# Kernel optimization log

Measured on AMD Instinct MI355X. Metric: run time of the kernel, lower is better.

## Reference

```python
import jax, jax.numpy as jnp
import numpy as np

EPS = 1e-6

def rmsnorm(x, w):
    # matches torch RMSNorm: normalize in fp32, cast back, scale
    xf = x.astype(jnp.float32)
    n = xf * jax.lax.rsqrt(jnp.mean(xf * xf, axis=-1, keepdims=True) + EPS)
    return n.astype(x.dtype) * w

def swiglu(x, w1, w2, w3):
    # torch Linear convention: weight shape [out, in], y = x @ W.T
    return (jax.nn.silu(x @ w1.T) * (x @ w3.T)) @ w2.T

B, D, E, K = 32768, 1024, 8, 2
NF = 4  # int(8 * 0.5) fractal experts, rest are plain SwiGLU(dim, 4*dim)

def setup_inputs() -> dict:
    key = jax.random.key(0)
    ks = jax.random.split(key, 8)
    def w(k, shape, fan_in):
        return jax.random.normal(k, shape, jnp.float32) * (fan_in ** -0.5)
    return {
        "x": jax.random.normal(ks[0], (B, D), jnp.float32),
        "gate_w": w(ks[1], (E, D), D),
        # FractalBlock experts (depth=1): RMSNorm weight, SwiGLU(dim, 2*dim), LayerScale gamma
        "fr_norm": jnp.ones((NF, D), jnp.float32),
        "fr_gamma": jnp.full((NF, D), 1e-5, jnp.float32),
        "fr_w1": w(ks[2], (NF, 2 * D, D), D),
        "fr_w2": w(ks[3], (NF, D, 2 * D), 2 * D),
        "fr_w3": w(ks[4], (NF, 2 * D, D), D),
        # Plain SwiGLU experts: SwiGLU(dim, 4*dim)
        "sw_w1": w(ks[5], (E - NF, 4 * D, D), D),
        "sw_w2": w(ks[6], (E - NF, D, 4 * D), 4 * D),
        "sw_w3": w(ks[7], (E - NF, 4 * D, D), D),
    }

def reference(x, gate_w, fr_norm, fr_gamma, fr_w1, fr_w2, fr_w3, sw_w1, sw_w2, sw_w3):
    n_experts = gate_w.shape[0]
    n_fractal = fr_w1.shape[0]
    # gating: softmax -> top-k -> renormalize selected weights
    probs = jax.nn.softmax(x @ gate_w.T, axis=-1)            # [B, E]
    tk_w, tk_i = jax.lax.top_k(probs, K)                     # [B, K]
    tk_w = tk_w / jnp.sum(tk_w, axis=-1, keepdims=True)
    # combine weights: zero for unselected experts (math identical to sparse dispatch)
    comb = jnp.sum(jax.nn.one_hot(tk_i, n_experts, dtype=x.dtype) * tk_w[..., None], axis=1)  # [B, E]
    out = jnp.zeros_like(x)
    for e in range(n_experts):  # fixed small structural loop over experts
        if e < n_fractal:
            # FractalBlock(depth=1), eval mode: stochastic depth is identity
            xn = rmsnorm(x, fr_norm[e])
            xn = xn + swiglu(xn, fr_w1[e], fr_w2[e], fr_w3[e])
            eo = fr_gamma[e] * xn + x
        else:
            j = e - n_fractal
            eo = swiglu(x, sw_w1[j], sw_w2[j], sw_w3[j])
        out = out + comb[:, e:e + 1] * eo
    return out
```

## Files before the change

### kernel.cpp

```cpp
#include <hip/hip_runtime.h>
#include <stdint.h>

#define B_TOK 32768
#define DIM   1024
#define NEXP  8
#define NFR   4
#define HF    2048
#define HS    4096
#define CT1   32
#define CT2   64
#define NCH   9
#define PADROWS 67584

typedef __bf16 bf16;
typedef bf16  bf16x8 __attribute__((ext_vector_type(8)));
typedef bf16  bf16x4 __attribute__((ext_vector_type(4)));
typedef float f32x4  __attribute__((ext_vector_type(4)));

#define LDSOFF(R, CC) (((R) << 6) + ((((CC) ^ ((R) & 7))) << 3))

__global__ __launch_bounds__(256) void gate_kernel(
    const float* __restrict__ x, const float* __restrict__ gw_g,
    bf16* __restrict__ xb, float* __restrict__ rms,
    int* __restrict__ top2, float* __restrict__ c12) {
  __shared__ float gw[NEXP * DIM];
  for (int i = threadIdx.x; i < NEXP * DIM / 4; i += 256)
    *(f32x4*)(gw + i * 4) = *(const f32x4*)(gw_g + i * 4);
  __syncthreads();
  const int lane = threadIdx.x & 63;
  const int wave = threadIdx.x >> 6;
  const int row  = blockIdx.x * 4 + wave;
  const float* xr = x + (size_t)row * DIM;
  f32x4 xv[4];
#pragma unroll
  for (int i = 0; i < 4; i++) xv[i] = *(const f32x4*)(xr + lane * 4 + i * 256);
  float ss = 0.f;
  double dot[8] = {0, 0, 0, 0, 0, 0, 0, 0};
#pragma unroll
  for (int i = 0; i < 4; i++) {
#pragma unroll
    for (int c = 0; c < 4; c++) ss += xv[i][c] * xv[i][c];
#pragma unroll
    for (int e = 0; e < 8; e++) {
      const f32x4 g = *(const f32x4*)(gw + e * DIM + i * 256 + lane * 4);
#pragma unroll
      for (int c = 0; c < 4; c++) dot[e] += (double)xv[i][c] * (double)g[c];
    }
  }
#pragma unroll
  for (int off = 32; off > 0; off >>= 1) {
    ss += __shfl_xor(ss, off, 64);
#pragma unroll
    for (int e = 0; e < 8; e++) dot[e] += __shfl_xor(dot[e], off, 64);
  }
  const float rv = 1.0f / sqrtf(ss * (1.0f / DIM) + 1e-6f);
  if (lane == 0) rms[row] = rv;
  int i1 = 0; double m1 = dot[0];
#pragma unroll
  for (int e = 1; e < 8; e++) if (dot[e] > m1) { m1 = dot[e]; i1 = e; }
  int i2 = 0; double m2 = -1e300;
#pragma unroll
  for (int e = 0; e < 8; e++) if (e != i1 && dot[e] > m2) { m2 = dot[e]; i2 = e; }
  const double t  = exp(m2 - m1);
  if (lane == 0) {
    top2[row] = i1 | (i2 << 8);
    c12[2 * row]     = (float)(1.0 / (1.0 + t));
    c12[2 * row + 1] = (float)(t / (1.0 + t));
  }
#pragma unroll
  for (int i = 0; i < 4; i++) {
    bf16x4 o;
#pragma unroll
    for (int c = 0; c < 4; c++) o[c] = (bf16)xv[i][c];
    *(bf16x4*)(xb + (size_t)row * DIM + lane * 4 + i * 256) = o;
  }
}

__global__ __launch_bounds__(1024) void histoff_kernel(
    const int* __restrict__ top2, int* __restrict__ tileOff256,
    int* __restrict__ tileOff128, int* __restrict__ rowOff) {
  __shared__ int h[8];
  if (threadIdx.x < 8) h[threadIdx.x] = 0;
  __syncthreads();
  int c[8] = {0, 0, 0, 0, 0, 0, 0, 0};
  for (int i = 0; i < B_TOK / 1024; i++) {
    const int pk = top2[threadIdx.x + i * 1024];
    const int e1 = pk & 255, e2 = pk >> 8;
#pragma unroll
    for (int e = 0; e < 8; e++) c[e] += (e1 == e) + (e2 == e);
  }
#pragma unroll
  for (int e = 0; e < 8; e++) {
#pragma unroll
    for (int off = 32; off > 0; off >>= 1) c[e] += __shfl_xor(c[e], off, 64);
  }
  if ((threadIdx.x & 63) == 0) {
#pragma unroll
    for (int e = 0; e < 8; e++) atomicAdd(&h[e], c[e]);
  }
  __syncthreads();
  if (threadIdx.x == 0) {
    int t = 0;
    for (int e = 0; e < 8; e++) {
      tileOff256[e] = t;
      tileOff128[e] = 2 * t;
      rowOff[e]     = t * 256;
      t += (h[e] + 255) >> 8;
    }
    tileOff256[8] = t;
    tileOff128[8] = 2 * t;
  }
}

__global__ __launch_bounds__(256) void assign_kernel(
    const int* __restrict__ top2, const float* __restrict__ c12,
    const int* __restrict__ rowOff, int* __restrict__ cur,
    int* __restrict__ perm, float* __restrict__ cwg) {
  __shared__ int lhist[8];
  __shared__ int lbase[8];
  if (threadIdx.x < 8) lhist[threadIdx.x] = 0;
  __syncthreads();
  const int t = blockIdx.x * 256 + threadIdx.x;
  const int pk = top2[t];
  const int e1 = pk & 255, e2 = pk >> 8;
  const int p1 = atomicAdd(&lhist[e1], 1);
  const int p2 = atomicAdd(&lhist[e2], 1);
  __syncthreads();
  if (threadIdx.x < 8) {
    const int c = lhist[threadIdx.x];
    lbase[threadIdx.x] = c ? atomicAdd(&cur[threadIdx.x * 32], c) : 0;
  }
  __syncthreads();
  const int g1 = rowOff[e1] + lbase[e1] + p1;
  perm[g1] = t; cwg[g1] = c12[2 * t];
  const int g2 = rowOff[e2] + lbase[e2] + p2;
  perm[g2] = t; cwg[g2] = c12[2 * t + 1];
}

__global__ __launch_bounds__(256) void cvt_kernel(
    const float* __restrict__ src, bf16* __restrict__ dst, int n4) {
  const int i = blockIdx.x * 256 + threadIdx.x;
  if (i >= n4) return;
  f32x4 v = *(const f32x4*)(src + (size_t)i * 4);
  *(bf16x4*)(dst + (size_t)i * 4) = __builtin_convertvector(v, bf16x4);
}

__global__ __launch_bounds__(256) void cvt_inter_fr(
    const float* __restrict__ w1, const float* __restrict__ w3,
    const float* __restrict__ norm, bf16* __restrict__ dst) {
  const int i = blockIdx.x * 256 + threadIdx.x;
  const int col4 = i & 255;
  const int rp   = (i >> 8) & 4095;
  const int e    = i >> 20;
  const int blk  = rp >> 4;
  const int sr   = ((blk >> 1) << 4) + (rp & 15);
  const float* src = (blk & 1) ? w3 : w1;
  f32x4 v  = *(const f32x4*)(src + ((size_t)e * HF + sr) * DIM + col4 * 4);
  f32x4 nv = *(const f32x4*)(norm + e * DIM + col4 * 4);
#pragma unroll
  for (int c = 0; c < 4; c++) v[c] *= nv[c];
  *(bf16x4*)(dst + ((size_t)e * 4096 + rp) * DIM + col4 * 4) =
      __builtin_convertvector(v, bf16x4);
}

__global__ __launch_bounds__(256) void cvt_inter_sw(
    const float* __restrict__ w1, const float* __restrict__ w3,
    bf16* __restrict__ dst) {
  const int i = blockIdx.x * 256 + threadIdx.x;
  const int col4 = i & 255;
  const int rp   = (i >> 8) & 8191;
  const int e    = i >> 21;
  const int blk  = rp >> 4;
  const int sr   = ((blk >> 1) << 4) + (rp & 15);
  const float* src = (blk & 1) ? w3 : w1;
  f32x4 v = *(const f32x4*)(src + ((size_t)e * HS + sr) * DIM + col4 * 4);
  *(bf16x4*)(dst + ((size_t)e * 8192 + rp) * DIM + col4 * 4) =
      __builtin_convertvector(v, bf16x4);
}

__device__ __forceinline__ void stage_sw(const bf16* __restrict__ g0, int ld,
                                         bf16* s0, int wave, int lane) {
  const int r = lane >> 3;
  const int c = (lane & 7) ^ r;
  const bf16* g = g0 + (size_t)(wave * 32 + r) * ld + c * 8;
  bf16* s = s0 + wave * 2048;
#pragma unroll
  for (int i = 0; i < 4; i++) {
    __builtin_amdgcn_global_load_lds(
        (const __attribute__((address_space(1))) void*)(uintptr_t)(g + (size_t)(i * 8) * ld),
        (__attribute__((address_space(3))) void*)(uintptr_t)(s + i * 512), 16, 0, 0);
  }
}

__global__ __launch_bounds__(512, 2) void gemm1_kernel(
    const bf16* __restrict__ xb, const int* __restrict__ perm,
    const float* __restrict__ rms,
    const bf16* __restrict__ fwi, const bf16* __restrict__ swi,
    const int* __restrict__ tileOff256, bf16* __restrict__ G, int chunk) {
  const int bt = chunk * CT1 + blockIdx.y;
  int toff[9];
#pragma unroll
  for (int i = 0; i < 9; i++) toff[i] = tileOff256[i];
  if (bt >= toff[8]) return;
  int e = 0;
#pragma unroll
  for (int i = 1; i < 8; i++) if (bt >= toff[i]) e = i;
  const bool isfr = (e < NFR);
  const int nt = isfr ? 16 : 32;
  if ((int)blockIdx.x >= nt) return;
  const bf16* Bp = isfr ? fwi + (size_t)e * 4096 * DIM
                        : swi + (size_t)(e - NFR) * 8192 * DIM;

  __shared__ __attribute__((aligned(16))) bf16 As[2 * 16384];
  __shared__ __attribute__((aligned(16))) bf16 Bs[2 * 16384];
  const int lane = threadIdx.x & 63, wave = threadIdx.x >> 6;
  const int wm = wave >> 2, wn = wave & 3;
  const int g0  = bt * 256;
  const int n0p = blockIdx.x * 256;

  const int rA = lane >> 3;
  const int cA = (lane & 7) ^ rA;
  const bf16* Ag[4];
#pragma unroll
  for (int i = 0; i < 4; i++) {
    int tk = perm[g0 + wave * 32 + i * 8 + rA];
    if (tk < 0) tk = 0;
    Ag[i] = xb + (size_t)tk * DIM + cA * 8;
  }
  const bf16* Bg = Bp + (size_t)(n0p + wave * 32 + rA) * DIM + cA * 8;

  f32x4 acc[8][4];
#pragma unroll
  for (int i = 0; i < 8; i++)
#pragma unroll
    for (int j = 0; j < 4; j++) { f32x4 z = {0.f, 0.f, 0.f, 0.f}; acc[i][j] = z; }
  const int lr = lane & 15, lq = lane >> 4;

  auto stage = [&](int buf, int k0) {
    bf16* sa = As + buf * 16384 + wave * 2048;
    bf16* sb = Bs + buf * 16384 + wave * 2048;
#pragma unroll
    for (int i = 0; i < 4; i++) {
      __builtin_amdgcn_global_load_lds(
          (const __attribute__((address_space(1))) void*)(uintptr_t)(Ag[i] + k0),
          (__attribute__((address_space(3))) void*)(uintptr_t)(sa + i * 512), 16, 0, 0);
    }
#pragma unroll
    for (int i = 0; i < 4; i++) {
      __builtin_amdgcn_global_load_lds(
          (const __attribute__((address_space(1))) void*)(uintptr_t)(Bg + (size_t)(i * 8) * DIM + k0),
          (__attribute__((address_space(3))) void*)(uintptr_t)(sb + i * 512), 16, 0, 0);
    }
  };
  auto compute = [&](int buf) {
    const bf16* Ab = As + buf * 16384;
    const bf16* Bb = Bs + buf * 16384;
#pragma unroll
    for (int ks = 0; ks < 2; ks++) {
      bf16x8 af[8], bfv[4];
#pragma unroll
      for (int mi = 0; mi < 8; mi++)
        af[mi] = *(const bf16x8*)(Ab + LDSOFF(wm * 128 + mi * 16 + lr, ks * 4 + lq));
#pragma unroll
      for (int ni = 0; ni < 4; ni++)
        bfv[ni] = *(const bf16x8*)(Bb + LDSOFF(wn * 64 + ni * 16 + lr, ks * 4 + lq));
      __builtin_amdgcn_s_setprio(1);
#pragma unroll
      for (int mi = 0; mi < 8; mi++)
#pragma unroll
        for (int ni = 0; ni < 4; ni++)
          acc[mi][ni] = __builtin_amdgcn_mfma_f32_16x16x32_bf16(af[mi], bfv[ni], acc[mi][ni], 0, 0, 0);
      __builtin_amdgcn_s_setprio(0);
    }
  };

  stage(0, 0);
  __syncthreads();
  int k = 64;
#pragma unroll 1
  for (int t = 0; t < 7; t++) {
    stage(1, k); compute(0); __syncthreads(); k += 64;
    stage(0, k); compute(1); __syncthreads(); k += 64;
  }
  stage(1, k); compute(0); __syncthreads();
  compute(1);

  const int gh = n0p >> 1;
#pragma unroll
  for (int mi = 0; mi < 8; mi++) {
#pragma unroll
    for (int r = 0; r < 4; r++) {
      const int row_l = wm * 128 + mi * 16 + lq * 4 + r;
      float s = 1.0f;
      if (isfr) {
        int tok = perm[g0 + row_l];
        s = rms[tok < 0 ? 0 : tok];
      }
      bf16* Grow = G + (size_t)(blockIdx.y * 256 + row_l) * HS;
#pragma unroll
      for (int nh = 0; nh < 2; nh++) {
        const float h1 = acc[mi][2 * nh][r] * s;
        const float h3 = acc[mi][2 * nh + 1][r] * s;
        const int col = gh + wn * 32 + nh * 16 + lr;
        Grow[col] = (bf16)(h1 / (1.0f + __expf(-h1)) * h3);
      }
    }
  }
}

__global__ __launch_bounds__(256, 2) void gemm2_kernel(
    const bf16* __restrict__ G, const int* __restrict__ perm,
    const float* __restrict__ cwg, const float* __restrict__ rms,
    const float* __restrict__ gamma_all, const float* __restrict__ norm_all,
    const float* __restrict__ x,
    const bf16* __restrict__ fw2, const bf16* __restrict__ s2b,
    const int* __restrict__ tileOff128, float* __restrict__ out, int chunk) {
  const int bt = chunk * CT2 + blockIdx.y;
  int toff[9];
#pragma unroll
  for (int i = 0; i < 9; i++) toff[i] = tileOff128[i];
  if (bt >= toff[8]) return;
  int e = 0;
#pragma unroll
  for (int i = 1; i < 8; i++) if (bt >= toff[i]) e = i;
  const bool isfr = (e < NFR);
  const int K = isfr ? HF : HS;
  const bf16* Bw = isfr ? fw2 + (size_t)e * DIM * HF : s2b + (size_t)(e - NFR) * DIM * HS;

  __shared__ __attribute__((aligned(16))) bf16 As[128 * 64];
  __shared__ __attribute__((aligned(16))) bf16 Bs[128 * 64];
  const int lane = threadIdx.x & 63, wave = threadIdx.x >> 6;
  const int wm = wave >> 1, wn = wave & 1;
  const int n0 = blockIdx.x * 128;
  f32x4 acc[4][4];
#pragma unroll
  for (int i = 0; i < 4; i++)
#pragma unroll
    for (int j = 0; j < 4; j++) { f32x4 z = {0.f, 0.f, 0.f, 0.f}; acc[i][j] = z; }
  const bf16* Ab = G + (size_t)(blockIdx.y * 128) * HS;
  const bf16* Bb = Bw + (size_t)n0 * K;
  const int lr = lane & 15, lq = lane >> 4;
  for (int k0 = 0; k0 < K; k0 += 64) {
    stage_sw(Ab + k0, HS, As, wave, lane);
    stage_sw(Bb + k0, K, Bs, wave, lane);
    __syncthreads();
#pragma unroll
    for (int ks = 0; ks < 2; ks++) {
      bf16x8 af[4], bf_[4];
#pragma unroll
      for (int mi = 0; mi < 4; mi++) {
        const int R = wm * 64 + mi * 16 + lr;
        af[mi] = *(const bf16x8*)(As + LDSOFF(R, ks * 4 + lq));
      }
#pragma unroll
      for (int ni = 0; ni < 4; ni++) {
        const int R = wn * 64 + ni * 16 + lr;
        bf_[ni] = *(const bf16x8*)(Bs + LDSOFF(R, ks * 4 + lq));
      }
#pragma unroll
      for (int mi = 0; mi < 4; mi++)
#pragma unroll
        for (int ni = 0; ni < 4; ni++)
          acc[mi][ni] = __builtin_amdgcn_mfma_f32_16x16x32_bf16(af[mi], bf_[ni], acc[mi][ni], 0, 0, 0);
    }
    __syncthreads();
  }
#pragma unroll
  for (int mi = 0; mi < 4; mi++) {
#pragma unroll
    for (int r = 0; r < 4; r++) {
      const int row_l = wm * 64 + mi * 16 + lq * 4 + r;
      const int g_row = bt * 128 + row_l;
      const int tok = perm[g_row];
      if (tok < 0) continue;
      const float cw = cwg[g_row];
      const float rv = rms[tok];
#pragma unroll
      for (int ni = 0; ni < 4; ni++) {
        const int col = n0 + wn * 64 + ni * 16 + lr;
        const float a = acc[mi][ni][r];
        float res;
        if (isfr) {
          const float xvv = x[(size_t)tok * DIM + col];
          res = cw * (gamma_all[e * DIM + col] * (rv * xvv * norm_all[e * DIM + col] + a) + xvv);
        } else {
          res = cw * a;
        }
        atomicAdd(&out[(size_t)tok * DIM + col], res);
      }
    }
  }
}

extern "C" void kernel_launch(void* const* d_in, const int* in_sizes, int n_in,
                              void* d_out, int out_size, void* d_ws, size_t ws_size,
                              hipStream_t stream) {
  const float* x        = (const float*)d_in[0];
  const float* gate_w   = (const float*)d_in[1];
  const float* fr_norm  = (const float*)d_in[2];
  const float* fr_gamma = (const float*)d_in[3];
  const float* fr_w1    = (const float*)d_in[4];
  const float* fr_w2    = (const float*)d_in[5];
  const float* fr_w3    = (const float*)d_in[6];
  const float* sw_w1    = (const float*)d_in[7];
  const float* sw_w2    = (const float*)d_in[8];
  const float* sw_w3    = (const float*)d_in[9];
  float* out = (float*)d_out;

  char* ws = (char*)d_ws;
  bf16*  xb    = (bf16*)(ws);
  bf16*  fwi   = (bf16*)(ws + 67108864);
  bf16*  fw2   = (bf16*)(ws + 100663296);
  bf16*  swi   = (bf16*)(ws + 117440512);
  bf16*  s2b   = (bf16*)(ws + 184549376);
  bf16*  G     = (bf16*)(ws + 218103808);
  float* rmsb  = (float*)(ws + 285212672);
  int*   top2  = (int*)  (ws + 285343744);
  float* c12   = (float*)(ws + 285474816);
  int*   perm  = (int*)  (ws + 285736960);
  float* cwg   = (float*)(ws + 286007296);
  int*   cur   = (int*)  (ws + 286277632);
  int*   tileOff256 = (int*)(ws + 286278656);
  int*   tileOff128 = (int*)(ws + 286278720);
  int*   rowOff     = (int*)(ws + 286278784);

  hipMemsetAsync(d_out, 0, (size_t)out_size * sizeof(float), stream);
  hipMemsetAsync(cur, 0, 1024, stream);
  hipMemsetAsync(perm, 0xFF, PADROWS * 4, stream);

  gate_kernel<<<B_TOK / 4, 256, 0, stream>>>(x, gate_w, xb, rmsb, top2, c12);
  histoff_kernel<<<1, 1024, 0, stream>>>(top2, tileOff256, tileOff128, rowOff);
  assign_kernel<<<B_TOK / 256, 256, 0, stream>>>(top2, c12, rowOff, cur, perm, cwg);

  cvt_inter_fr<<<16384, 256, 0, stream>>>(fr_w1, fr_w3, fr_norm, fwi);
  cvt_kernel<<<8192, 256, 0, stream>>>(fr_w2, fw2, 2097152);
  cvt_inter_sw<<<32768, 256, 0, stream>>>(sw_w1, sw_w3, swi);
  cvt_kernel<<<16384, 256, 0, stream>>>(sw_w2, s2b, 4194304);

  for (int c = 0; c < NCH; c++) {
    gemm1_kernel<<<dim3(32, CT1), 512, 0, stream>>>(
        xb, perm, rmsb, fwi, swi, tileOff256, G, c);
    gemm2_kernel<<<dim3(8, CT2), 256, 0, stream>>>(
        G, perm, cwg, rmsb, fr_gamma, fr_norm, x, fw2, s2b, tileOff128, out, c);
  }
}
```

Measured before the change: 2.728 ms.

## Double-buffer LDS in down-projection GEMM and relax barriers to vmcnt waits

The second (down-projection) GEMM kernel moves from a single LDS buffer with two __syncthreads per K step to a double-buffered ping-pong scheme. The next tile's global loads are issued before computing on the current tile, and MFMA blocks are wrapped in s_setprio. Both GEMM kernels also replace __syncthreads with an explicit vmcnt(0) wait plus a raw s_barrier, and the first kernel's loop is folded into one 15-iteration loop. This aims to overlap global-to-LDS staging with matrix math, at the cost of doubling LDS use (64KB per block), which may reduce occupancy. Skipping the lgkmcnt wait relies on the stage path using direct-to-LDS or register-staged loads that vmcnt alone covers.

```diff
diff --git a/kernel.cpp b/kernel.cpp
--- a/kernel.cpp
+++ b/kernel.cpp
@@ -275,14 +275,16 @@
   };
 
   stage(0, 0);
-  __syncthreads();
-  int k = 64;
+  asm volatile("s_waitcnt vmcnt(0)" ::: "memory");
+  __builtin_amdgcn_s_barrier();
 #pragma unroll 1
-  for (int t = 0; t < 7; t++) {
-    stage(1, k); compute(0); __syncthreads(); k += 64;
-    stage(0, k); compute(1); __syncthreads(); k += 64;
-  }
-  stage(1, k); compute(0); __syncthreads();
+  for (int t = 0; t < 15; t++) {
+    const int cur = t & 1;
+    stage(cur ^ 1, (t + 1) * 64);
+    compute(cur);
+    asm volatile("s_waitcnt vmcnt(0)" ::: "memory");
+    __builtin_amdgcn_s_barrier();
+  }
   compute(1);
 
   const int gh = n0p >> 1;
@@ -327,8 +329,8 @@
   const int K = isfr ? HF : HS;
   const bf16* Bw = isfr ? fw2 + (size_t)e * DIM * HF : s2b + (size_t)(e - NFR) * DIM * HS;
 
-  __shared__ __attribute__((aligned(16))) bf16 As[128 * 64];
-  __shared__ __attribute__((aligned(16))) bf16 Bs[128 * 64];
+  __shared__ __attribute__((aligned(16))) bf16 As[2 * 8192];
+  __shared__ __attribute__((aligned(16))) bf16 Bs[2 * 8192];
   const int lane = threadIdx.x & 63, wave = threadIdx.x >> 6;
   const int wm = wave >> 1, wn = wave & 1;
   const int n0 = blockIdx.x * 128;
@@ -340,31 +342,46 @@
   const bf16* Ab = G + (size_t)(blockIdx.y * 128) * HS;
   const bf16* Bb = Bw + (size_t)n0 * K;
   const int lr = lane & 15, lq = lane >> 4;
-  for (int k0 = 0; k0 < K; k0 += 64) {
-    stage_sw(Ab + k0, HS, As, wave, lane);
-    stage_sw(Bb + k0, K, Bs, wave, lane);
-    __syncthreads();
+
+  auto compute = [&](int buf) {
+    const bf16* Ap = As + buf * 8192;
+    const bf16* Bp = Bs + buf * 8192;
 #pragma unroll
     for (int ks = 0; ks < 2; ks++) {
       bf16x8 af[4], bf_[4];
 #pragma unroll
-      for (int mi = 0; mi < 4; mi++) {
-        const int R = wm * 64 + mi * 16 + lr;
-        af[mi] = *(const bf16x8*)(As + LDSOFF(R, ks * 4 + lq));
-      }
-#pragma unroll
-      for (int ni = 0; ni < 4; ni++) {
-        const int R = wn * 64 + ni * 16 + lr;
-        bf_[ni] = *(const bf16x8*)(Bs + LDSOFF(R, ks * 4 + lq));
-      }
+      for (int mi = 0; mi < 4; mi++)
+        af[mi] = *(const bf16x8*)(Ap + LDSOFF(wm * 64 + mi * 16 + lr, ks * 4 + lq));
+#pragma unroll
+      for (int ni = 0; ni < 4; ni++)
+        bf_[ni] = *(const bf16x8*)(Bp + LDSOFF(wn * 64 + ni * 16 + lr, ks * 4 + lq));
+      __builtin_amdgcn_s_setprio(1);
 #pragma unroll
       for (int mi = 0; mi < 4; mi++)
 #pragma unroll
         for (int ni = 0; ni < 4; ni++)
           acc[mi][ni] = __builtin_amdgcn_mfma_f32_16x16x32_bf16(af[mi], bf_[ni], acc[mi][ni], 0, 0, 0);
-    }
-    __syncthreads();
-  }
+      __builtin_amdgcn_s_setprio(0);
+    }
+  };
+
+  stage_sw(Ab, HS, As, wave, lane);
+  stage_sw(Bb, K, Bs, wave, lane);
+  asm volatile("s_waitcnt vmcnt(0)" ::: "memory");
+  __builtin_amdgcn_s_barrier();
+  const int NTK = K >> 6;
+#pragma unroll 1
+  for (int t = 0; t < NTK - 1; t++) {
+    const int cur = t & 1;
+    const int k1 = (t + 1) << 6;
+    stage_sw(Ab + k1, HS, As + (cur ^ 1) * 8192, wave, lane);
+    stage_sw(Bb + k1, K, Bs + (cur ^ 1) * 8192, wave, lane);
+    compute(cur);
+    asm volatile("s_waitcnt vmcnt(0)" ::: "memory");
+    __builtin_amdgcn_s_barrier();
+  }
+  compute((NTK - 1) & 1);
+
 #pragma unroll
   for (int mi = 0; mi < 4; mi++) {
 #pragma unroll
```

New measurement: 2.642 ms. -3.2%, faster.
